# Optimization experiments

Measured on AMD Instinct MI355X. Metric: run time of the kernel, lower is better.

The kernel has to match this reference:

```python
import jax, jax.numpy as jnp
import numpy as np
from jax import lax

SAMPLES = 1024
RADIUS = 0.2
MAX_NEIGHBORS = 32


def setup_inputs() -> dict:
    key = jax.random.key(0)
    k1, k2 = jax.random.split(key)
    B, N, C = 4, 16384, 128
    xyz = jax.random.uniform(k1, (B, N, 3), dtype=jnp.float32)       # points in unit cube
    features = jax.random.normal(k2, (B, N, C), dtype=jnp.float32)
    return {"xyz": xyz, "features": features}


def farthest_point_sample(xyz, n_samples):
    """xyz: [B,N,3] -> indices [B,S] (iterative max of running min-distance)."""
    B, N, _ = xyz.shape
    first = jnp.zeros((B,), dtype=jnp.int32)

    def step(carry, _):
        min_d, last = carry                                   # [B,N], [B]
        last_pt = jnp.take_along_axis(xyz, last[:, None, None], axis=1)  # [B,1,3]
        d = jnp.sum((xyz - last_pt) ** 2, axis=-1)            # [B,N]
        min_d = jnp.minimum(min_d, d)
        nxt = jnp.argmax(min_d, axis=1).astype(jnp.int32)     # [B]
        return (min_d, nxt), nxt

    init = (jnp.full((B, N), 1e10, dtype=jnp.float32), first)
    _, rest = lax.scan(step, init, None, length=n_samples - 1)  # [S-1,B]
    return jnp.concatenate([first[None], rest], axis=0).T        # [B,S]


def ball_query(centroids, xyz, features, radius, k):
    """centroids: [B,S,3]; xyz: [B,N,3]; features: [B,N,C].
    Returns grouped xyz (centered) [B,S,K,3] and grouped features [B,S,K,C].
    Takes the first K in-radius points (by index order), padding with the
    first valid index -- matching the PointNet++ CUDA ball_query kernel."""
    B, N, _ = xyz.shape
    sqd = jnp.sum((centroids[:, :, None, :] - xyz[:, None, :, :]) ** 2, axis=-1)  # [B,S,N]
    in_ball = sqd <= radius * radius
    scores = jnp.where(in_ball, jnp.arange(N, dtype=jnp.int32), N)  # smaller = earlier valid idx
    neg_vals, idx = lax.top_k(-scores, k)                           # K smallest scores
    valid = (-neg_vals) < N                                          # [B,S,K]
    idx = jnp.where(valid, idx, idx[..., :1])                        # pad with first hit
    b = jnp.arange(B)[:, None, None]
    grouped_xyz = xyz[b, idx] - centroids[:, :, None, :]             # [B,S,K,3]
    grouped_feat = features[b, idx]                                  # [B,S,K,C]
    return grouped_xyz, grouped_feat


def reference(xyz, features):
    fps_idx = farthest_point_sample(xyz, SAMPLES)                    # [B,S]
    b = jnp.arange(xyz.shape[0])[:, None]
    centroids = lax.stop_gradient(xyz[b, fps_idx])                   # [B,S,3] (torch.no_grad)
    grouped_xyz, grouped_feat = ball_query(centroids, xyz, features, RADIUS, MAX_NEIGHBORS)
    return centroids, grouped_xyz, grouped_feat
```

## Files before the change

### kernel.cpp

```cpp
#include <hip/hip_runtime.h>
#include <cstdint>
#include <cstddef>

#define NPTS 16384
#define NSAMP 1024
#define KNBR 32
#define NCH 128


#define FPS_TPB 512

typedef float f32x2 __attribute__((ext_vector_type(2)));

#define PR16_FOREACH(X) \
  X(0) X(1) X(2) X(3) X(4) X(5) X(6) X(7) \
  X(8) X(9) X(10) X(11) X(12) X(13) X(14) X(15)

__global__ __launch_bounds__(FPS_TPB)
__attribute__((amdgpu_waves_per_eu(2, 2)))
void fps_kernel(
    const float* __restrict__ xyz, float* __restrict__ centroids) {
#pragma clang fp contract(off)
  const int b = blockIdx.x;
  const int t = threadIdx.x;
  const float* __restrict__ px = xyz + (size_t)b * NPTS * 3;

#define DECL_PR(j) f32x2 X##j, Y##j, Z##j, M##j;
  PR16_FOREACH(DECL_PR)
#undef DECL_PR

#define LOAD_PR(j)                                  \
  {                                                 \
    const int pa = (2 * (j)) * FPS_TPB + t;         \
    const int pb = pa + FPS_TPB;                    \
    X##j.x = px[pa * 3 + 0];                        \
    Y##j.x = px[pa * 3 + 1];                        \
    Z##j.x = px[pa * 3 + 2];                        \
    X##j.y = px[pb * 3 + 0];                        \
    Y##j.y = px[pb * 3 + 1];                        \
    Z##j.y = px[pb * 3 + 2];                        \
    M##j = {1e10f, 1e10f};                          \
  }
  PR16_FOREACH(LOAD_PR)
#undef LOAD_PR

  __shared__ unsigned long long s_wkey[2][FPS_TPB / 64];

  float* co = centroids + (size_t)b * NSAMP * 3;
  float lx = px[0], ly = px[1], lz = px[2];
  if (t == 0) { co[0] = lx; co[1] = ly; co[2] = lz; }

  for (int s = 1; s < NSAMP; ++s) {
    const int par = s & 1;
    const f32x2 cx = {lx, lx};
    const f32x2 cy = {ly, ly};
    const f32x2 cz = {lz, lz};

    float bv = -1.0f;
    int bs = 0;
#define UPD_PR(j)                                                       \
    {                                                                   \
      f32x2 dx = X##j - cx, dy = Y##j - cy, dz = Z##j - cz;             \
      f32x2 dd = (dx * dx + dy * dy) + dz * dz;             \
      M##j.x = fminf(M##j.x, dd.x);                                     \
      M##j.y = fminf(M##j.y, dd.y);                                     \
      float vj; int sj;                                                 \
      if (M##j.y > M##j.x) { vj = M##j.y; sj = 2 * (j) + 1; }           \
      else                 { vj = M##j.x; sj = 2 * (j); }               \
      if (vj > bv) { bv = vj; bs = sj; }       \
    }
    PR16_FOREACH(UPD_PR)
#undef UPD_PR

    const unsigned int bi = ((unsigned int)bs << 9) | (unsigned int)t;
    unsigned long long key =
        ((unsigned long long)__float_as_uint(bv) << 32) |
        (unsigned int)(~bi);

#pragma unroll
    for (int off = 1; off < 64; off <<= 1) {
      const unsigned long long ok = __shfl_xor(key, off);
      if (ok > key) key = ok;
    }
    if ((t & 63) == 0) s_wkey[par][t >> 6] = key;
    __syncthreads();

    unsigned long long best = s_wkey[par][0];
#pragma unroll
    for (int w = 1; w < FPS_TPB / 64; ++w) {
      const unsigned long long k2 = s_wkey[par][w];
      if (k2 > best) best = k2;
    }
    const unsigned int widx =
        (unsigned int)__builtin_amdgcn_readfirstlane((int)(~(unsigned int)best));

    lx = px[widx * 3 + 0];
    ly = px[widx * 3 + 1];
    lz = px[widx * 3 + 2];
    if (t == 0) {
      co[s * 3 + 0] = lx;
      co[s * 3 + 1] = ly;
      co[s * 3 + 2] = lz;
    }
  }
}

__global__ __launch_bounds__(256) void group_kernel(
    const float* __restrict__ xyz, const float* __restrict__ feat,
    const float* __restrict__ centroids,
    float* __restrict__ gxyz, float* __restrict__ gfeat) {
#pragma clang fp contract(off)
  const int wave = threadIdx.x >> 6;
  const int lane = threadIdx.x & 63;
  const int gw = blockIdx.x * 4 + wave;
  const int b = gw >> 10;

  const float* px = xyz + (size_t)b * NPTS * 3;
  const float* pc = centroids + (size_t)gw * 3;
  const float cx = pc[0], cy = pc[1], cz = pc[2];
  const float rr = 0.04f;

  __shared__ int sh_idx[4][KNBR];
  __shared__ float sh_gx[4][KNBR * 3];

  int cnt = 0;
  for (int n0 = 0; n0 < NPTS && cnt < KNBR; n0 += 64) {
    const int p = n0 + lane;
    const float xx = px[p * 3 + 0];
    const float yy = px[p * 3 + 1];
    const float zz = px[p * 3 + 2];
    const float dx = xx - cx;
    const float dy = yy - cy;
    const float dz = zz - cz;
    const float d = (dx * dx + dy * dy) + dz * dz;
    const bool in = d <= rr;
    const unsigned long long mask = __ballot(in);
    const int pos = cnt + (int)__popcll(mask & ((1ull << lane) - 1ull));
    if (in && pos < KNBR) {
      sh_idx[wave][pos] = p;
      sh_gx[wave][pos * 3 + 0] = dx;
      sh_gx[wave][pos * 3 + 1] = dy;
      sh_gx[wave][pos * 3 + 2] = dz;
    }
    cnt += (int)__popcll(mask);
  }
  if (cnt == 0 && lane == 0) {
    sh_idx[wave][0] = 0;
    sh_gx[wave][0] = px[0] - cx;
    sh_gx[wave][1] = px[1] - cy;
    sh_gx[wave][2] = px[2] - cz;
  }
  const int nf0 = (cnt < 1) ? 1 : cnt;
  const int nf = (nf0 < KNBR) ? nf0 : KNBR;
  __syncthreads();
  if (lane < KNBR && lane >= nf) {
    sh_idx[wave][lane] = sh_idx[wave][0];
    sh_gx[wave][lane * 3 + 0] = sh_gx[wave][0];
    sh_gx[wave][lane * 3 + 1] = sh_gx[wave][1];
    sh_gx[wave][lane * 3 + 2] = sh_gx[wave][2];
  }
  __syncthreads();

  float* ox = gxyz + (size_t)gw * KNBR * 3;
  const float* shf = sh_gx[wave];
  for (int j = lane; j < KNBR * 3; j += 64) ox[j] = shf[j];

  float* og = gfeat + (size_t)gw * KNBR * NCH;
  const float* pf = feat + (size_t)b * NPTS * NCH;
#pragma unroll 4
  for (int k = 0; k < KNBR; ++k) {
    const int row = sh_idx[wave][k];
    const float2 v = ((const float2*)(pf + (size_t)row * NCH))[lane];
    ((float2*)(og + (size_t)k * NCH))[lane] = v;
  }
}

extern "C" void kernel_launch(void* const* d_in, const int* in_sizes, int n_in,
                              void* d_out, int out_size, void* d_ws, size_t ws_size,
                              hipStream_t stream) {
  const float* xyz = (const float*)d_in[0];
  const float* feat = (const float*)d_in[1];
  float* out = (float*)d_out;
  const int B = in_sizes[0] / (NPTS * 3);

  float* centroids = out;
  float* gxyz = centroids + (size_t)B * NSAMP * 3;
  float* gfeat = gxyz + (size_t)B * NSAMP * KNBR * 3;

  fps_kernel<<<B, FPS_TPB, 0, stream>>>(xyz, centroids);
  group_kernel<<<(B * NSAMP) / 4, 256, 0, stream>>>(xyz, feat, centroids, gxyz,
                                                    gfeat);
}
```

Measured before the change: 1.830 ms.

## Fuse FPS and grouping into one persistent kernel with progress-flag overlap

Merges farthest point sampling and ball-query grouping into a single launch. B blocks run FPS and publish a per-batch progress counter after each step, while the other 16*B blocks spin-wait on that counter and group each centroid as soon as it is ready. Grouping therefore overlaps the long serial FPS loop instead of running after it. The FPS distance math is also rewritten in inline packed-float asm. The risks are spin-wait overhead, relaxed-ordering memory visibility, a deadlock guard that could yield wrong results if it expires, and dependence on all blocks being co-resident.

After: 2.169 ms. +18.5%, slower.

```diff
diff --git a/kernel.cpp b/kernel.cpp
--- a/kernel.cpp
+++ b/kernel.cpp
@@ -9,12 +9,226 @@
 
 
 #define FPS_TPB 512
+#define PROG_STRIDE 32
 
 typedef float f32x2 __attribute__((ext_vector_type(2)));
 
 #define PR16_FOREACH(X) \
   X(0) X(1) X(2) X(3) X(4) X(5) X(6) X(7) \
   X(8) X(9) X(10) X(11) X(12) X(13) X(14) X(15)
+
+__global__ void init_progress(unsigned* __restrict__ p, int n) {
+  const int i = blockIdx.x * blockDim.x + threadIdx.x;
+  if (i < n) p[i] = 0u;
+}
+
+__global__ __launch_bounds__(FPS_TPB)
+__attribute__((amdgpu_waves_per_eu(2, 2)))
+void fused_kernel(const float* __restrict__ xyz, const float* __restrict__ feat,
+                  float* __restrict__ centroids, float* __restrict__ gxyz,
+                  float* __restrict__ gfeat, unsigned* __restrict__ progress,
+                  int B) {
+#pragma clang fp contract(off)
+  __shared__ unsigned long long s_wkey[2][FPS_TPB / 64];
+  __shared__ int sh_idx[8][KNBR];
+  __shared__ float sh_gx[8][KNBR * 3];
+
+  if ((int)blockIdx.x < B) {
+    const int b = blockIdx.x;
+    const int t = threadIdx.x;
+    const float* __restrict__ px = xyz + (size_t)b * NPTS * 3;
+    float* co = centroids + (size_t)b * NSAMP * 3;
+    unsigned* prog = progress + b * PROG_STRIDE;
+
+#define DECL_PR(j) f32x2 X##j, Y##j, Z##j, M##j;
+    PR16_FOREACH(DECL_PR)
+#undef DECL_PR
+
+#define LOAD_PR(j)                                  \
+    {                                               \
+      const int pa = (2 * (j)) * FPS_TPB + t;       \
+      const int pb = pa + FPS_TPB;                  \
+      X##j.x = px[pa * 3 + 0];                      \
+      Y##j.x = px[pa * 3 + 1];                      \
+      Z##j.x = px[pa * 3 + 2];                      \
+      X##j.y = px[pb * 3 + 0];                      \
+      Y##j.y = px[pb * 3 + 1];                      \
+      Z##j.y = px[pb * 3 + 2];                      \
+      M##j = {1e10f, 1e10f};                        \
+    }
+    PR16_FOREACH(LOAD_PR)
+#undef LOAD_PR
+
+    float lx = px[0], ly = px[1], lz = px[2];
+    if (t == 0) {
+      __hip_atomic_store((unsigned*)&co[0], __float_as_uint(lx),
+                         __ATOMIC_RELAXED, __HIP_MEMORY_SCOPE_AGENT);
+      __hip_atomic_store((unsigned*)&co[1], __float_as_uint(ly),
+                         __ATOMIC_RELAXED, __HIP_MEMORY_SCOPE_AGENT);
+      __hip_atomic_store((unsigned*)&co[2], __float_as_uint(lz),
+                         __ATOMIC_RELAXED, __HIP_MEMORY_SCOPE_AGENT);
+    }
+
+    for (int s = 1; s < NSAMP; ++s) {
+      const int par = s & 1;
+      const f32x2 cx = {lx, lx};
+      const f32x2 cy = {ly, ly};
+      const f32x2 cz = {lz, lz};
+
+      float bv = -1.0f;
+      int bs = 0;
+#define UPD_PR(j)                                                         \
+      {                                                                   \
+        f32x2 dx, dy, dz, sx, sy, sz, s1, s2;                             \
+        asm("v_pk_add_f32 %0, %1, %2 neg_lo:[0,1] neg_hi:[0,1]"           \
+            : "=v"(dx) : "v"(X##j), "v"(cx));                             \
+        asm("v_pk_add_f32 %0, %1, %2 neg_lo:[0,1] neg_hi:[0,1]"           \
+            : "=v"(dy) : "v"(Y##j), "v"(cy));                             \
+        asm("v_pk_add_f32 %0, %1, %2 neg_lo:[0,1] neg_hi:[0,1]"           \
+            : "=v"(dz) : "v"(Z##j), "v"(cz));                             \
+        asm("v_pk_mul_f32 %0, %1, %1" : "=v"(sx) : "v"(dx));              \
+        asm("v_pk_mul_f32 %0, %1, %1" : "=v"(sy) : "v"(dy));              \
+        asm("v_pk_mul_f32 %0, %1, %1" : "=v"(sz) : "v"(dz));              \
+        asm("v_pk_add_f32 %0, %1, %2" : "=v"(s1) : "v"(sx), "v"(sy));     \
+        asm("v_pk_add_f32 %0, %1, %2" : "=v"(s2) : "v"(s1), "v"(sz));     \
+        M##j.x = fminf(M##j.x, s2.x);                                     \
+        M##j.y = fminf(M##j.y, s2.y);                                     \
+        float vj; int sj;                                                 \
+        if (M##j.y > M##j.x) { vj = M##j.y; sj = 2 * (j) + 1; }           \
+        else                 { vj = M##j.x; sj = 2 * (j); }               \
+        if (vj > bv) { bv = vj; bs = sj; }       \
+      }
+      PR16_FOREACH(UPD_PR)
+#undef UPD_PR
+
+      const unsigned int bi = ((unsigned int)bs << 9) | (unsigned int)t;
+      unsigned long long key =
+          ((unsigned long long)__float_as_uint(bv) << 32) |
+          (unsigned int)(~bi);
+
+#pragma unroll
+      for (int off = 1; off < 64; off <<= 1) {
+        const unsigned long long ok = __shfl_xor(key, off);
+        if (ok > key) key = ok;
+      }
+      if ((t & 63) == 0) s_wkey[par][t >> 6] = key;
+      __syncthreads();
+
+      if (t == 0)
+        __hip_atomic_store(prog, (unsigned)s, __ATOMIC_RELAXED,
+                           __HIP_MEMORY_SCOPE_AGENT);
+
+      unsigned long long best = s_wkey[par][0];
+#pragma unroll
+      for (int w = 1; w < FPS_TPB / 64; ++w) {
+        const unsigned long long k2 = s_wkey[par][w];
+        if (k2 > best) best = k2;
+      }
+      const unsigned int widx = (unsigned int)__builtin_amdgcn_readfirstlane(
+          (int)(~(unsigned int)best));
+
+      lx = px[widx * 3 + 0];
+      ly = px[widx * 3 + 1];
+      lz = px[widx * 3 + 2];
+      if (t == 0) {
+        __hip_atomic_store((unsigned*)&co[s * 3 + 0], __float_as_uint(lx),
+                           __ATOMIC_RELAXED, __HIP_MEMORY_SCOPE_AGENT);
+        __hip_atomic_store((unsigned*)&co[s * 3 + 1], __float_as_uint(ly),
+                           __ATOMIC_RELAXED, __HIP_MEMORY_SCOPE_AGENT);
+        __hip_atomic_store((unsigned*)&co[s * 3 + 2], __float_as_uint(lz),
+                           __ATOMIC_RELAXED, __HIP_MEMORY_SCOPE_AGENT);
+      }
+    }
+    __syncthreads();
+    if (t == 0)
+      __hip_atomic_store(prog, (unsigned)NSAMP, __ATOMIC_RELAXED,
+                         __HIP_MEMORY_SCOPE_AGENT);
+  } else {
+    const int gi = blockIdx.x - B;
+    const int wave = threadIdx.x >> 6;
+    const int lane = threadIdx.x & 63;
+    const int w = gi * 8 + wave;
+    const int WPB = B * 128;
+    const float rr = 0.04f;
+
+    for (int i = 0; i < 8; ++i) {
+      const int gw = w + WPB * i;
+      const int b = gw >> 10;
+      const int s = gw & 1023;
+      unsigned* prog = progress + b * PROG_STRIDE;
+
+      unsigned pr = __hip_atomic_load(prog, __ATOMIC_RELAXED,
+                                      __HIP_MEMORY_SCOPE_AGENT);
+      int g = 0;
+      while (pr < (unsigned)(s + 1) && g < (1 << 20)) {
+        __builtin_amdgcn_s_sleep(16);
+        pr = __hip_atomic_load(prog, __ATOMIC_RELAXED,
+                               __HIP_MEMORY_SCOPE_AGENT);
+        ++g;
+      }
+
+      const float* px = xyz + (size_t)b * NPTS * 3;
+      const float* pc = centroids + (size_t)gw * 3;
+      const float cx = __uint_as_float(__hip_atomic_load(
+          (const unsigned*)&pc[0], __ATOMIC_RELAXED, __HIP_MEMORY_SCOPE_AGENT));
+      const float cy = __uint_as_float(__hip_atomic_load(
+          (const unsigned*)&pc[1], __ATOMIC_RELAXED, __HIP_MEMORY_SCOPE_AGENT));
+      const float cz = __uint_as_float(__hip_atomic_load(
+          (const unsigned*)&pc[2], __ATOMIC_RELAXED, __HIP_MEMORY_SCOPE_AGENT));
+
+      int cnt = 0;
+      for (int n0 = 0; n0 < NPTS && cnt < KNBR; n0 += 64) {
+        const int p = n0 + lane;
+        const float xx = px[p * 3 + 0];
+        const float yy = px[p * 3 + 1];
+        const float zz = px[p * 3 + 2];
+        const float dx = xx - cx;
+        const float dy = yy - cy;
+        const float dz = zz - cz;
+        const float d = (dx * dx + dy * dy) + dz * dz;
+        const bool in = d <= rr;
+        const unsigned long long mask = __ballot(in);
+        const int pos = cnt + (int)__popcll(mask & ((1ull << lane) - 1ull));
+        if (in && pos < KNBR) {
+          sh_idx[wave][pos] = p;
+          sh_gx[wave][pos * 3 + 0] = dx;
+          sh_gx[wave][pos * 3 + 1] = dy;
+          sh_gx[wave][pos * 3 + 2] = dz;
+        }
+        cnt += (int)__popcll(mask);
+      }
+      if (cnt == 0 && lane == 0) {
+        sh_idx[wave][0] = 0;
+        sh_gx[wave][0] = px[0] - cx;
+        sh_gx[wave][1] = px[1] - cy;
+        sh_gx[wave][2] = px[2] - cz;
+      }
+      const int nf0 = (cnt < 1) ? 1 : cnt;
+      const int nf = (nf0 < KNBR) ? nf0 : KNBR;
+      __syncthreads();
+      if (lane < KNBR && lane >= nf) {
+        sh_idx[wave][lane] = sh_idx[wave][0];
+        sh_gx[wave][lane * 3 + 0] = sh_gx[wave][0];
+        sh_gx[wave][lane * 3 + 1] = sh_gx[wave][1];
+        sh_gx[wave][lane * 3 + 2] = sh_gx[wave][2];
+      }
+      __syncthreads();
+
+      float* ox = gxyz + (size_t)gw * KNBR * 3;
+      const float* shf = sh_gx[wave];
+      for (int j = lane; j < KNBR * 3; j += 64) ox[j] = shf[j];
+
+      float* og = gfeat + (size_t)gw * KNBR * NCH;
+      const float* pf = feat + (size_t)b * NPTS * NCH;
+#pragma unroll 4
+      for (int k = 0; k < KNBR; ++k) {
+        const int row = sh_idx[wave][k];
+        const float2 v = ((const float2*)(pf + (size_t)row * NCH))[lane];
+        ((float2*)(og + (size_t)k * NCH))[lane] = v;
+      }
+    }
+  }
+}
 
 __global__ __launch_bounds__(FPS_TPB)
 __attribute__((amdgpu_waves_per_eu(2, 2)))
@@ -28,7 +242,6 @@
 #define DECL_PR(j) f32x2 X##j, Y##j, Z##j, M##j;
   PR16_FOREACH(DECL_PR)
 #undef DECL_PR
-
 #define LOAD_PR(j)                                  \
   {                                                 \
     const int pa = (2 * (j)) * FPS_TPB + t;         \
@@ -45,7 +258,6 @@
 #undef LOAD_PR
 
   __shared__ unsigned long long s_wkey[2][FPS_TPB / 64];
-
   float* co = centroids + (size_t)b * NSAMP * 3;
   float lx = px[0], ly = px[1], lz = px[2];
   if (t == 0) { co[0] = lx; co[1] = ly; co[2] = lz; }
@@ -55,28 +267,25 @@
     const f32x2 cx = {lx, lx};
     const f32x2 cy = {ly, ly};
     const f32x2 cz = {lz, lz};
-
     float bv = -1.0f;
     int bs = 0;
 #define UPD_PR(j)                                                       \
     {                                                                   \
       f32x2 dx = X##j - cx, dy = Y##j - cy, dz = Z##j - cz;             \
-      f32x2 dd = (dx * dx + dy * dy) + dz * dz;             \
+      f32x2 dd = (dx * dx + dy * dy) + dz * dz;                         \
       M##j.x = fminf(M##j.x, dd.x);                                     \
       M##j.y = fminf(M##j.y, dd.y);                                     \
       float vj; int sj;                                                 \
       if (M##j.y > M##j.x) { vj = M##j.y; sj = 2 * (j) + 1; }           \
       else                 { vj = M##j.x; sj = 2 * (j); }               \
-      if (vj > bv) { bv = vj; bs = sj; }       \
+      if (vj > bv) { bv = vj; bs = sj; }                                \
     }
     PR16_FOREACH(UPD_PR)
 #undef UPD_PR
-
     const unsigned int bi = ((unsigned int)bs << 9) | (unsigned int)t;
     unsigned long long key =
         ((unsigned long long)__float_as_uint(bv) << 32) |
         (unsigned int)(~bi);
-
 #pragma unroll
     for (int off = 1; off < 64; off <<= 1) {
       const unsigned long long ok = __shfl_xor(key, off);
@@ -84,16 +293,14 @@
     }
     if ((t & 63) == 0) s_wkey[par][t >> 6] = key;
     __syncthreads();
-
     unsigned long long best = s_wkey[par][0];
 #pragma unroll
     for (int w = 1; w < FPS_TPB / 64; ++w) {
       const unsigned long long k2 = s_wkey[par][w];
       if (k2 > best) best = k2;
     }
-    const unsigned int widx =
-        (unsigned int)__builtin_amdgcn_readfirstlane((int)(~(unsigned int)best));
-
+    const unsigned int widx = (unsigned int)__builtin_amdgcn_readfirstlane(
+        (int)(~(unsigned int)best));
     lx = px[widx * 3 + 0];
     ly = px[widx * 3 + 1];
     lz = px[widx * 3 + 2];
@@ -114,7 +321,6 @@
   const int lane = threadIdx.x & 63;
   const int gw = blockIdx.x * 4 + wave;
   const int b = gw >> 10;
-
   const float* px = xyz + (size_t)b * NPTS * 3;
   const float* pc = centroids + (size_t)gw * 3;
   const float cx = pc[0], cy = pc[1], cz = pc[2];
@@ -160,11 +366,9 @@
     sh_gx[wave][lane * 3 + 2] = sh_gx[wave][2];
   }
   __syncthreads();
-
   float* ox = gxyz + (size_t)gw * KNBR * 3;
   const float* shf = sh_gx[wave];
   for (int j = lane; j < KNBR * 3; j += 64) ox[j] = shf[j];
-
   float* og = gfeat + (size_t)gw * KNBR * NCH;
   const float* pf = feat + (size_t)b * NPTS * NCH;
 #pragma unroll 4
@@ -187,7 +391,16 @@
   float* gxyz = centroids + (size_t)B * NSAMP * 3;
   float* gfeat = gxyz + (size_t)B * NSAMP * KNBR * 3;
 
-  fps_kernel<<<B, FPS_TPB, 0, stream>>>(xyz, centroids);
-  group_kernel<<<(B * NSAMP) / 4, 256, 0, stream>>>(xyz, feat, centroids, gxyz,
-                                                    gfeat);
+  const int nprog = B * PROG_STRIDE;
+  const size_t need = (size_t)nprog * sizeof(unsigned);
+  if (d_ws != nullptr && ws_size >= need) {
+    unsigned* progress = (unsigned*)d_ws;
+    init_progress<<<(nprog + 127) / 128, 128, 0, stream>>>(progress, nprog);
+    fused_kernel<<<B * 17, FPS_TPB, 0, stream>>>(xyz, feat, centroids, gxyz,
+                                                 gfeat, progress, B);
+  } else {
+    fps_kernel<<<B, FPS_TPB, 0, stream>>>(xyz, centroids);
+    group_kernel<<<(B * NSAMP) / 4, 256, 0, stream>>>(xyz, feat, centroids,
+                                                      gxyz, gfeat);
+  }
 }
```

## Double FPS block size and give each centroid its own group block

Applied to the files above, without the earlier changes.

The FPS kernel now runs 1024 threads per batch with 16 points per thread instead of 32. The cross-wave reduction replaces the serial shared-memory scan with a shuffle-xor tree over 16 wave keys. The grouping kernel now maps one centroid to a 256-thread block: wave 0 does the ball query and all four waves split the feature gather. The aim is to shorten the serial per-iteration FPS critical path and to spread the gather across more waves, at the cost of more block-wide syncs and three idle waves during the ball query.

Result: slower. 2.000 ms (+9.2%).

```diff
diff --git a/kernel.cpp b/kernel.cpp
--- a/kernel.cpp
+++ b/kernel.cpp
@@ -8,25 +8,26 @@
 #define NCH 128
 
 
-#define FPS_TPB 512
+#define FPS_TPB 1024
+#define FPS_WAVES (FPS_TPB / 64)
 
 typedef float f32x2 __attribute__((ext_vector_type(2)));
 
-#define PR16_FOREACH(X) \
-  X(0) X(1) X(2) X(3) X(4) X(5) X(6) X(7) \
-  X(8) X(9) X(10) X(11) X(12) X(13) X(14) X(15)
+#define PR8_FOREACH(X) X(0) X(1) X(2) X(3) X(4) X(5) X(6) X(7)
 
 __global__ __launch_bounds__(FPS_TPB)
-__attribute__((amdgpu_waves_per_eu(2, 2)))
+__attribute__((amdgpu_waves_per_eu(4, 4)))
 void fps_kernel(
     const float* __restrict__ xyz, float* __restrict__ centroids) {
 #pragma clang fp contract(off)
   const int b = blockIdx.x;
   const int t = threadIdx.x;
+  const int lane = t & 63;
+  const int wave = t >> 6;
   const float* __restrict__ px = xyz + (size_t)b * NPTS * 3;
 
 #define DECL_PR(j) f32x2 X##j, Y##j, Z##j, M##j;
-  PR16_FOREACH(DECL_PR)
+  PR8_FOREACH(DECL_PR)
 #undef DECL_PR
 
 #define LOAD_PR(j)                                  \
@@ -41,10 +42,10 @@
     Z##j.y = px[pb * 3 + 2];                        \
     M##j = {1e10f, 1e10f};                          \
   }
-  PR16_FOREACH(LOAD_PR)
+  PR8_FOREACH(LOAD_PR)
 #undef LOAD_PR
 
-  __shared__ unsigned long long s_wkey[2][FPS_TPB / 64];
+  __shared__ unsigned long long s_wkey[2][FPS_WAVES];
 
   float* co = centroids + (size_t)b * NSAMP * 3;
   float lx = px[0], ly = px[1], lz = px[2];
@@ -69,10 +70,10 @@
       else                 { vj = M##j.x; sj = 2 * (j); }               \
       if (vj > bv) { bv = vj; bs = sj; }       \
     }
-    PR16_FOREACH(UPD_PR)
+    PR8_FOREACH(UPD_PR)
 #undef UPD_PR
 
-    const unsigned int bi = ((unsigned int)bs << 9) | (unsigned int)t;
+    const unsigned int bi = ((unsigned int)bs << 10) | (unsigned int)t;
     unsigned long long key =
         ((unsigned long long)__float_as_uint(bv) << 32) |
         (unsigned int)(~bi);
@@ -82,17 +83,17 @@
       const unsigned long long ok = __shfl_xor(key, off);
       if (ok > key) key = ok;
     }
-    if ((t & 63) == 0) s_wkey[par][t >> 6] = key;
+    if (lane == 0) s_wkey[par][wave] = key;
     __syncthreads();
 
-    unsigned long long best = s_wkey[par][0];
+    unsigned long long best = s_wkey[par][lane & 15];
 #pragma unroll
-    for (int w = 1; w < FPS_TPB / 64; ++w) {
-      const unsigned long long k2 = s_wkey[par][w];
-      if (k2 > best) best = k2;
+    for (int off = 1; off < 16; off <<= 1) {
+      const unsigned long long ok = __shfl_xor(best, off);
+      if (ok > best) best = ok;
     }
-    const unsigned int widx =
-        (unsigned int)__builtin_amdgcn_readfirstlane((int)(~(unsigned int)best));
+    const unsigned int widx = (unsigned int)__builtin_amdgcn_readfirstlane(
+        (int)(~(unsigned int)best));
 
     lx = px[widx * 3 + 0];
     ly = px[widx * 3 + 1];
@@ -110,66 +111,69 @@
     const float* __restrict__ centroids,
     float* __restrict__ gxyz, float* __restrict__ gfeat) {
 #pragma clang fp contract(off)
+  const int gw = blockIdx.x;
+  const int b = gw >> 10;
   const int wave = threadIdx.x >> 6;
   const int lane = threadIdx.x & 63;
-  const int gw = blockIdx.x * 4 + wave;
-  const int b = gw >> 10;
 
   const float* px = xyz + (size_t)b * NPTS * 3;
   const float* pc = centroids + (size_t)gw * 3;
   const float cx = pc[0], cy = pc[1], cz = pc[2];
   const float rr = 0.04f;
 
-  __shared__ int sh_idx[4][KNBR];
-  __shared__ float sh_gx[4][KNBR * 3];
+  __shared__ int sh_idx[KNBR];
+  __shared__ float sh_gx[KNBR * 3];
+  __shared__ int sh_cnt;
 
-  int cnt = 0;
-  for (int n0 = 0; n0 < NPTS && cnt < KNBR; n0 += 64) {
-    const int p = n0 + lane;
-    const float xx = px[p * 3 + 0];
-    const float yy = px[p * 3 + 1];
-    const float zz = px[p * 3 + 2];
-    const float dx = xx - cx;
-    const float dy = yy - cy;
-    const float dz = zz - cz;
-    const float d = (dx * dx + dy * dy) + dz * dz;
-    const bool in = d <= rr;
-    const unsigned long long mask = __ballot(in);
-    const int pos = cnt + (int)__popcll(mask & ((1ull << lane) - 1ull));
-    if (in && pos < KNBR) {
-      sh_idx[wave][pos] = p;
-      sh_gx[wave][pos * 3 + 0] = dx;
-      sh_gx[wave][pos * 3 + 1] = dy;
-      sh_gx[wave][pos * 3 + 2] = dz;
+  if (wave == 0) {
+    int cnt = 0;
+    for (int n0 = 0; n0 < NPTS && cnt < KNBR; n0 += 64) {
+      const int p = n0 + lane;
+      const float xx = px[p * 3 + 0];
+      const float yy = px[p * 3 + 1];
+      const float zz = px[p * 3 + 2];
+      const float dx = xx - cx;
+      const float dy = yy - cy;
+      const float dz = zz - cz;
+      const float d = (dx * dx + dy * dy) + dz * dz;
+      const bool in = d <= rr;
+      const unsigned long long mask = __ballot(in);
+      const int pos = cnt + (int)__popcll(mask & ((1ull << lane) - 1ull));
+      if (in && pos < KNBR) {
+        sh_idx[pos] = p;
+        sh_gx[pos * 3 + 0] = dx;
+        sh_gx[pos * 3 + 1] = dy;
+        sh_gx[pos * 3 + 2] = dz;
+      }
+      cnt += (int)__popcll(mask);
     }
-    cnt += (int)__popcll(mask);
+    if (cnt == 0 && lane == 0) {
+      sh_idx[0] = 0;
+      sh_gx[0] = px[0] - cx;
+      sh_gx[1] = px[1] - cy;
+      sh_gx[2] = px[2] - cz;
+    }
+    if (lane == 0) sh_cnt = (cnt < 1) ? 1 : cnt;
   }
-  if (cnt == 0 && lane == 0) {
-    sh_idx[wave][0] = 0;
-    sh_gx[wave][0] = px[0] - cx;
-    sh_gx[wave][1] = px[1] - cy;
-    sh_gx[wave][2] = px[2] - cz;
-  }
-  const int nf0 = (cnt < 1) ? 1 : cnt;
-  const int nf = (nf0 < KNBR) ? nf0 : KNBR;
   __syncthreads();
-  if (lane < KNBR && lane >= nf) {
-    sh_idx[wave][lane] = sh_idx[wave][0];
-    sh_gx[wave][lane * 3 + 0] = sh_gx[wave][0];
-    sh_gx[wave][lane * 3 + 1] = sh_gx[wave][1];
-    sh_gx[wave][lane * 3 + 2] = sh_gx[wave][2];
+
+  const int nf = (sh_cnt < KNBR) ? sh_cnt : KNBR;
+  if ((int)threadIdx.x < KNBR && (int)threadIdx.x >= nf) {
+    sh_idx[threadIdx.x] = sh_idx[0];
+    sh_gx[threadIdx.x * 3 + 0] = sh_gx[0];
+    sh_gx[threadIdx.x * 3 + 1] = sh_gx[1];
+    sh_gx[threadIdx.x * 3 + 2] = sh_gx[2];
   }
   __syncthreads();
 
   float* ox = gxyz + (size_t)gw * KNBR * 3;
-  const float* shf = sh_gx[wave];
-  for (int j = lane; j < KNBR * 3; j += 64) ox[j] = shf[j];
+  if (threadIdx.x < KNBR * 3) ox[threadIdx.x] = sh_gx[threadIdx.x];
 
   float* og = gfeat + (size_t)gw * KNBR * NCH;
   const float* pf = feat + (size_t)b * NPTS * NCH;
-#pragma unroll 4
-  for (int k = 0; k < KNBR; ++k) {
-    const int row = sh_idx[wave][k];
+#pragma unroll
+  for (int k = wave; k < KNBR; k += 4) {
+    const int row = sh_idx[k];
     const float2 v = ((const float2*)(pf + (size_t)row * NCH))[lane];
     ((float2*)(og + (size_t)k * NCH))[lane] = v;
   }
@@ -188,6 +192,6 @@
   float* gfeat = gxyz + (size_t)B * NSAMP * KNBR * 3;
 
   fps_kernel<<<B, FPS_TPB, 0, stream>>>(xyz, centroids);
-  group_kernel<<<(B * NSAMP) / 4, 256, 0, stream>>>(xyz, feat, centroids, gxyz,
-                                                    gfeat);
+  group_kernel<<<B * NSAMP, 256, 0, stream>>>(xyz, feat, centroids, gxyz,
+                                              gfeat);
 }
```
